# Optimization experiments

Hardware: AMD Instinct MI355X
Metric: run time of the kernel (lower is better)

The kernel has to match this reference:

```python
import jax, jax.numpy as jnp
import numpy as np


def setup_inputs() -> dict:
    key = jax.random.key(0)
    ks = jax.random.split(key, 8)
    B, S, H = 16, 512, 1024
    K, E, L = 32, 1024, 2  # max_node_length, max_edge_length=K**2, num_labels
    seq = jax.random.normal(ks[0], (B, S, H), jnp.float32)
    # structured cumulative proof offsets: col0=1 ('<s>' offset, skipped by forward),
    # then n increasing offsets, zeros terminate. n <= K-1 so NAF node fits in K slots.
    rng = np.random.default_rng(0)
    off = np.zeros((B, K), np.int64)
    off[:, 0] = 1
    for b in range(B):
        n = int(rng.integers(8, K))  # 8..31 segment nodes
        lens = rng.integers(4, 14, size=n)
        off[b, 1:n + 1] = np.cumsum(lens)  # max < 31*13+1 < S
    s = 0.02
    w = lambda k, shp: jax.random.normal(k, shp, jnp.float32) * s
    return {
        'sequence_outputs': seq,
        'proof_offsets': jnp.asarray(off),
        'naf_W': w(ks[1], (H, H)), 'naf_b': jnp.zeros((H,), jnp.float32),
        'cls_dense_W': w(ks[2], (H, H)), 'cls_dense_b': jnp.zeros((H,), jnp.float32),
        'cls_out_W': w(ks[3], (H, L)), 'cls_out_b': jnp.zeros((L,), jnp.float32),
        'node_dense_W': w(ks[4], (H, H)), 'node_dense_b': jnp.zeros((H,), jnp.float32),
        'node_out_W': w(ks[5], (H, L)), 'node_out_b': jnp.zeros((L,), jnp.float32),
        'edge_dense_W': w(ks[6], (3 * H, H)), 'edge_dense_b': jnp.zeros((H,), jnp.float32),
        'edge_out_W': w(ks[7], (H, L)), 'edge_out_b': jnp.zeros((L,), jnp.float32),
        'max_node_length': K,
        'max_edge_length': E,
    }


def _head(x, dW, db, oW, ob):
    # dropout is identity in eval mode
    return jnp.tanh(x @ dW + db) @ oW + ob


def reference(sequence_outputs, proof_offsets,
              naf_W, naf_b, cls_dense_W, cls_dense_b, cls_out_W, cls_out_b,
              node_dense_W, node_dense_b, node_out_W, node_out_b,
              edge_dense_W, edge_dense_b, edge_out_W, edge_out_b,
              max_node_length, max_edge_length):
    B, S, H = sequence_outputs.shape
    K = max_node_length
    E = max_edge_length
    cls_tok = sequence_outputs[:, 0, :]                      # [B,H]
    naf = cls_tok @ naf_W + naf_b                            # [B,H]
    logits = _head(cls_tok, cls_dense_W, cls_dense_b, cls_out_W, cls_out_b)  # [B,L]

    # segment-mean pooling over variable-length spans
    off = proof_offsets[:, 1:]                               # [B,K-1] cumulative offsets
    valid = off > 0                                          # [B,K-1]
    n = valid.sum(axis=1)                                    # [B] #segment nodes
    starts = jnp.concatenate([jnp.ones((B, 1), off.dtype), off[:, :-1] + 1], axis=1)
    pos = jnp.arange(S)
    mask = ((pos[None, None, :] >= starts[:, :, None])
            & (pos[None, None, :] <= off[:, :, None])
            & valid[:, :, None]).astype(sequence_outputs.dtype)  # [B,K-1,S]
    sums = jnp.einsum('bks,bsh->bkh', mask, sequence_outputs)
    counts = mask.sum(axis=-1, keepdims=True)
    node_emb = sums / jnp.maximum(counts, 1.0)               # [B,K-1,H]

    # place segment nodes in slots [0,n), NAF at slot n, zeros after (padded batch buffer)
    slots = jnp.arange(K)
    is_naf = slots[None, :] == n[:, None]
    is_node = slots[None, :] < n[:, None]
    node_emb_p = jnp.pad(node_emb, ((0, 0), (0, 1), (0, 0)))  # [B,K,H]
    full_nodes = jnp.where(is_naf[:, :, None], naf[:, None, :],
                           jnp.where(is_node[:, :, None], node_emb_p, 0.0))  # [B,K,H]

    node_logits = _head(full_nodes, node_dense_W, node_dense_b, node_out_W, node_out_b)

    # pairwise edge features, row-major flattened per sample with m=n+1 nodes:
    # edge[i*m+j] = [node[j], node[i], node[j]-node[i]]
    m = n + 1                                                # [B]
    e = jnp.arange(E)
    i_idx = e[None, :] // m[:, None]                         # [B,E]
    j_idx = e[None, :] % m[:, None]
    valid_e = e[None, :] < (m * m)[:, None]
    i_c = jnp.clip(i_idx, 0, K - 1)
    j_c = jnp.clip(j_idx, 0, K - 1)
    ni = jnp.take_along_axis(full_nodes, i_c[:, :, None], axis=1)  # [B,E,H]
    nj = jnp.take_along_axis(full_nodes, j_c[:, :, None], axis=1)
    edge_feat = jnp.where(valid_e[:, :, None],
                          jnp.concatenate([nj, ni, nj - ni], axis=-1), 0.0)  # [B,E,3H]

    edge_logits = _head(edge_feat, edge_dense_W, edge_dense_b, edge_out_W, edge_out_b)

    return logits, node_logits, edge_logits
```

## Files before the change

### kernel.cpp

```cpp
#include <hip/hip_runtime.h>
#include <hip/hip_bf16.h>

typedef __hip_bfloat16 bf16;
typedef unsigned short ushort;
typedef __attribute__((ext_vector_type(8))) short short8v;
typedef __attribute__((ext_vector_type(4))) float float4v;

__device__ __forceinline__ float us2f(unsigned int u) {
    union { unsigned int i; float f; } c; c.i = u << 16; return c.f;
}
__device__ __forceinline__ bf16 f2bf(float x) { return __float2bfloat16(x); }
__device__ __forceinline__ ushort f2bfu(float x) {
    union { float f; unsigned int i; } c; c.f = x;
    unsigned int lsb = (c.i >> 16) & 1;
    return (ushort)((c.i + 0x7FFF + lsb) >> 16);
}
__device__ __forceinline__ float fcf(float x) {
    return fminf(1000.f, fmaxf(-1000.f, x));
}
__device__ __forceinline__ int iclamp(int v, int lo, int hi) {
    return v < lo ? lo : (v > hi ? hi : v);
}

__device__ __forceinline__ int po_ps(const int* po) {
    return ((po[1] | po[3] | po[5]) == 0) ? 2 : 1;
}
__device__ __forceinline__ int count_n(const int* po, int b, int ps) {
    int n = 0;
    #pragma unroll
    for (int j = 1; j < 32; ++j) n += (po[(b * 32 + j) * ps] > 0) ? 1 : 0;
    return iclamp(n, 0, 31);
}

__global__ __launch_bounds__(256) void k_sentinel(float* __restrict__ out, int nv, float val) {
    int i = blockIdx.x * 256 + threadIdx.x;
    if (i < nv) out[i] = val;
}


__device__ __forceinline__ void dev_prep(int kt, int nt, int z, int tid,
                                         const float* __restrict__ ndW,
                                         const float* __restrict__ eW,
                                         ushort* __restrict__ Wct, float* smemf)
{
    float (*T)[33] = (float (*)[33])smemf;

    const int k_loc = tid >> 3, n0 = (tid & 7) * 4;
    const size_t gofs = (size_t)(kt * 32 + k_loc) * 1024 + nt * 32 + n0;
    float4 v;
    if (z == 0) {
        v = *(const float4*)(ndW + gofs);
    } else if (z == 1) {
        float4 a = *(const float4*)(eW + gofs);
        float4 b = *(const float4*)(eW + (size_t)2048 * 1024 + gofs);
        v = make_float4(a.x + b.x, a.y + b.y, a.z + b.z, a.w + b.w);
    } else {
        float4 a = *(const float4*)(eW + (size_t)1024 * 1024 + gofs);
        float4 b = *(const float4*)(eW + (size_t)2048 * 1024 + gofs);
        v = make_float4(a.x - b.x, a.y - b.y, a.z - b.z, a.w - b.w);
    }
    T[k_loc][n0 + 0] = v.x; T[k_loc][n0 + 1] = v.y;
    T[k_loc][n0 + 2] = v.z; T[k_loc][n0 + 3] = v.w;
    __syncthreads();

    const int n_loc = tid >> 3, k0 = (tid & 7) * 4;
    ushort* dst = Wct + (size_t)z * 1024 * 1024 + (size_t)(nt * 32 + n_loc) * 1024 + kt * 32 + k0;
    ushort4 o;
    o.x = f2bfu(T[k0 + 0][n_loc]); o.y = f2bfu(T[k0 + 1][n_loc]);
    o.z = f2bfu(T[k0 + 2][n_loc]); o.w = f2bfu(T[k0 + 3][n_loc]);
    *(ushort4*)dst = o;
}

__device__ __forceinline__ void dev_nodes(int bx, int tid,
                                          const float* __restrict__ seq,
                                          const int* __restrict__ po,
                                          bf16* __restrict__ fn, int bbase)
{
    const int b_loc = bx >> 5;
    const int k = bx & 31;
    const int b = bbase + b_loc;
    const int ps = po_ps(po);
    const int n = count_n(po, b, ps);
    if (k == n) return;

    const int h0 = tid * 4;
    float4 acc = make_float4(0.f, 0.f, 0.f, 0.f);
    if (k < n) {
        int s_end   = iclamp(po[(b * 32 + k + 1) * ps], 1, 511);
        int s_begin = (k == 0) ? 1 : iclamp(po[(b * 32 + k) * ps] + 1, 1, 511);
        if (s_end < s_begin) s_end = s_begin;
        const float inv = 1.0f / (float)(s_end - s_begin + 1);
        float4 acc2 = make_float4(0.f, 0.f, 0.f, 0.f);
        int s = s_begin;
        const float* base = seq + (size_t)b * 524288 + h0;
        for (; s + 1 <= s_end; s += 2) {
            float4 u = *(const float4*)(base + (size_t)s * 1024);
            float4 v = *(const float4*)(base + (size_t)(s + 1) * 1024);
            acc.x += u.x;  acc.y += u.y;  acc.z += u.z;  acc.w += u.w;
            acc2.x += v.x; acc2.y += v.y; acc2.z += v.z; acc2.w += v.w;
        }
        if (s <= s_end) {
            float4 u = *(const float4*)(base + (size_t)s * 1024);
            acc.x += u.x; acc.y += u.y; acc.z += u.z; acc.w += u.w;
        }
        acc.x = (acc.x + acc2.x) * inv; acc.y = (acc.y + acc2.y) * inv;
        acc.z = (acc.z + acc2.z) * inv; acc.w = (acc.w + acc2.w) * inv;
    }
    bf16* dst = fn + (size_t)(b_loc * 32 + k) * 1024 + h0;
    dst[0] = f2bf(acc.x); dst[1] = f2bf(acc.y); dst[2] = f2bf(acc.z); dst[3] = f2bf(acc.w);
}

__device__ __forceinline__ void dev_cls(int b_loc, int q, int tid,
                                        const float* __restrict__ seq,
                                        const int* __restrict__ po,
                                        const float* __restrict__ nafW, const float* __restrict__ nafb,
                                        const float* __restrict__ clsW, const float* __restrict__ clsb,
                                        const float* __restrict__ clsoW,
                                        bf16* __restrict__ fn,
                                        float* __restrict__ cacc,
                                        int bbase, float* smemf)
{
    const int b = bbase + b_loc;
    float* xs   = smemf;
    float* redc = smemf + 1024;
    float* redn = smemf + 2048;
    for (int j = tid; j < 1024; j += 256) xs[j] = seq[(size_t)b * 524288 + j];
    __syncthreads();

    const int c16 = tid & 15, kq = tid >> 4;
    const int col0 = q * 64 + c16 * 4;
    const int kb = kq * 64;
    const float* wc_base = clsW + (size_t)kb * 1024 + col0;
    const float* wn_base = nafW + (size_t)kb * 1024 + col0;
    float4 ac = make_float4(0.f, 0.f, 0.f, 0.f);
    float4 an = make_float4(0.f, 0.f, 0.f, 0.f);
    #pragma unroll 4
    for (int i = 0; i < 64; ++i) {
        const float x = xs[kb + i];
        float4 wc = *(const float4*)(wc_base + (size_t)i * 1024);
        float4 wn = *(const float4*)(wn_base + (size_t)i * 1024);
        ac.x = fmaf(x, wc.x, ac.x); ac.y = fmaf(x, wc.y, ac.y);
        ac.z = fmaf(x, wc.z, ac.z); ac.w = fmaf(x, wc.w, ac.w);
        an.x = fmaf(x, wn.x, an.x); an.y = fmaf(x, wn.y, an.y);
        an.z = fmaf(x, wn.z, an.z); an.w = fmaf(x, wn.w, an.w);
    }
    *(float4*)&redc[kq * 64 + c16 * 4] = ac;
    *(float4*)&redn[kq * 64 + c16 * 4] = an;
    __syncthreads();

    if (tid < 64) {
        const int cl = tid;
        float cs = 0.f, ns = 0.f;
        #pragma unroll
        for (int kk = 0; kk < 16; ++kk) {
            cs += redc[kk * 64 + cl];
            ns += redn[kk * 64 + cl];
        }
        const int hout = q * 64 + cl;
        const int ps = po_ps(po);
        const int n = count_n(po, b, ps);
        fn[(size_t)(b_loc * 32 + n) * 1024 + hout] = f2bf(ns + nafb[hout]);
        float h = tanhf(cs + clsb[hout]);
        float2 ow = ((const float2*)clsoW)[hout];
        float q0 = h * ow.x, q1 = h * ow.y;
        #pragma unroll
        for (int off = 32; off > 0; off >>= 1) {
            q0 += __shfl_down(q0, off, 64);
            q1 += __shfl_down(q1, off, 64);
        }
        if (cl == 0) {
            cacc[(b_loc * 16 + q) * 2 + 0] = q0;
            cacc[(b_loc * 16 + q) * 2 + 1] = q1;
        }
    }
}

__device__ __forceinline__ void dev_econ(int tid,
                                         const float* __restrict__ edb,
                                         const float* __restrict__ eoW,
                                         float* __restrict__ econ)
{
    if (tid >= 64) return;
    const int lane = tid;
    float a0 = 0.f, a1 = 0.f;
    #pragma unroll
    for (int c = 0; c < 16; ++c) {
        const int idx = c * 64 + lane;
        float t = tanhf(edb[idx]);
        float2 ow = ((const float2*)eoW)[idx];
        a0 = fmaf(t, ow.x, a0);
        a1 = fmaf(t, ow.y, a1);
    }
    #pragma unroll
    for (int off = 32; off > 0; off >>= 1) {
        a0 += __shfl_down(a0, off, 64);
        a1 += __shfl_down(a1, off, 64);
    }
    if (lane == 0) { econ[0] = a0; econ[1] = a1; }
}

__global__ __launch_bounds__(256) void k_fusedA(const float* __restrict__ seq,
                                                const int* __restrict__ po,
                                                const float* __restrict__ nafW, const float* __restrict__ nafb,
                                                const float* __restrict__ clsW, const float* __restrict__ clsb,
                                                const float* __restrict__ clsoW,
                                                const float* __restrict__ ndW,
                                                const float* __restrict__ eW,
                                                const float* __restrict__ edb,
                                                const float* __restrict__ eoW,
                                                bf16* __restrict__ fn,
                                                float* __restrict__ cacc,
                                                ushort* __restrict__ Wct,
                                                float* __restrict__ econ)
{
    __shared__ __align__(16) float smem[3072];
    const int blk = blockIdx.x;
    const int tid = threadIdx.x;
    if (blk < 256) {
        dev_cls(blk & 15, blk >> 4, tid, seq, po, nafW, nafb, clsW, clsb, clsoW, fn, cacc, 0, smem);
    } else if (blk < 768) {
        dev_nodes(blk - 256, tid, seq, po, fn, 0);
    } else if (blk < 3840) {
        const int rem = blk - 768;
        const int z = rem >> 10, t10 = rem & 1023;
        dev_prep(t10 & 31, t10 >> 5, z, tid, ndW, eW, Wct, smem);
    } else {
        dev_econ(tid, edb, eoW, econ);
    }
}

__global__ __launch_bounds__(256) void k_nodes(const float* __restrict__ seq,
                                               const int* __restrict__ po,
                                               bf16* __restrict__ fn, int bbase)
{
    dev_nodes(blockIdx.x, threadIdx.x, seq, po, fn, bbase);
}
__global__ __launch_bounds__(256) void k_cls(const float* __restrict__ seq,
                                             const int* __restrict__ po,
                                             const float* __restrict__ nafW, const float* __restrict__ nafb,
                                             const float* __restrict__ clsW, const float* __restrict__ clsb,
                                             const float* __restrict__ clsoW,
                                             bf16* __restrict__ fn,
                                             float* __restrict__ cacc, int bbase)
{
    __shared__ __align__(16) float smem[3072];
    dev_cls(blockIdx.x, blockIdx.y, threadIdx.x, seq, po, nafW, nafb, clsW, clsb, clsoW, fn, cacc, bbase, smem);
}

__global__ __launch_bounds__(256) void k_huv_mfma(const bf16* __restrict__ X,
                                                  const ushort* __restrict__ Wct,
                                                  const float* __restrict__ ndb,
                                                  const float* __restrict__ noW,
                                                  float* __restrict__ nacc,
                                                  bf16* __restrict__ U,
                                                  bf16* __restrict__ V)
{
    const int rt = blockIdx.x;
    const int cc = blockIdx.y;
    const int z  = blockIdx.z;
    const int tid = threadIdx.x;
    const int w = tid >> 6, lane = tid & 63;
    const int quad = lane >> 4, l16 = lane & 15;
    const int rbase = rt * 16;

    __shared__ char smem[32768];
    short* A_lds = (short*)smem;
    float* Rs    = (float*)smem;

    {
        const int r = tid >> 4, s = tid & 15;
        const ushort* src = (const ushort*)X + (size_t)(rbase + r) * 1024 + s * 64;
        #pragma unroll
        for (int cch = 0; cch < 8; ++cch) {
            const int k0 = s * 64 + cch * 8;
            uint4 v = *(const uint4*)(src + cch * 8);
            const int slot = ((k0 >> 5) * 64 + ((k0 >> 3) & 3) * 16 + r) * 8;
            *(uint4*)&A_lds[slot] = v;
        }
    }
    __syncthreads();

    const ushort* Wz = Wct + (size_t)z * 1024 * 1024;
    const int nbase = cc * 128 + w * 32;
    const ushort* B0 = Wz + (size_t)(nbase + l16) * 1024 + quad * 8;
    const ushort* B1 = B0 + (size_t)16 * 1024;

    float4v acc0 = {0.f, 0.f, 0.f, 0.f};
    float4v acc1 = {0.f, 0.f, 0.f, 0.f};

    #pragma unroll 4
    for (int ks = 0; ks < 1024; ks += 32) {
        short8v a  = *(const short8v*)&A_lds[((ks >> 5) * 64 + quad * 16 + l16) * 8];
        short8v b0 = *(const short8v*)(B0 + ks);
        short8v b1 = *(const short8v*)(B1 + ks);
        acc0 = __builtin_amdgcn_mfma_f32_16x16x32_bf16(a, b0, acc0, 0, 0, 0);
        acc1 = __builtin_amdgcn_mfma_f32_16x16x32_bf16(a, b1, acc1, 0, 0, 0);
    }
    __syncthreads();

    #pragma unroll
    for (int reg = 0; reg < 4; ++reg) {
        Rs[(quad * 4 + reg) * 128 + w * 32 + l16]      = acc0[reg];
        Rs[(quad * 4 + reg) * 128 + w * 32 + 16 + l16] = acc1[reg];
    }
    __syncthreads();

    const int row = tid >> 4;
    const int c0 = (tid & 15) * 8;
    const int gcol0 = cc * 128 + c0;
    const float* src = &Rs[row * 128 + c0];
    float s[8];
    {
        float4 a = ((const float4*)src)[0];
        float4 b = ((const float4*)src)[1];
        s[0] = a.x; s[1] = a.y; s[2] = a.z; s[3] = a.w;
        s[4] = b.x; s[5] = b.y; s[6] = b.z; s[7] = b.w;
    }
    if (z == 0) {
        float q0 = 0.f, q1 = 0.f;
        #pragma unroll
        for (int e = 0; e < 8; ++e) {
            float t = tanhf(s[e] + ndb[gcol0 + e]);
            float2 ow = ((const float2*)noW)[gcol0 + e];
            q0 = fmaf(t, ow.x, q0);
            q1 = fmaf(t, ow.y, q1);
        }
        #pragma unroll
        for (int off = 8; off > 0; off >>= 1) {
            q0 += __shfl_down(q0, off, 16);
            q1 += __shfl_down(q1, off, 16);
        }
        if ((tid & 15) == 0) {
            float* np = nacc + ((size_t)(rbase + row) * 8 + cc) * 2;
            np[0] = q0; np[1] = q1;
        }
    } else {
        bf16* dstbuf = (z == 1) ? U : V;
        bf16* dst = dstbuf + (size_t)(rbase + row) * 1024 + gcol0;
        #pragma unroll
        for (int e = 0; e < 8; ++e) dst[e] = f2bf(s[e]);
    }
}

__global__ __launch_bounds__(256) void k_huv_valu(const bf16* __restrict__ X,
                                                  const float* __restrict__ ndW, const float* __restrict__ ndb,
                                                  const float* __restrict__ noW,
                                                  const float* __restrict__ eW,
                                                  float* __restrict__ nacc,
                                                  bf16* __restrict__ U,
                                                  bf16* __restrict__ V)
{
    const int rt = blockIdx.x, cc = blockIdx.y, z = blockIdx.z;
    const int tid = threadIdx.x;
    const int w = tid >> 6, lane = tid & 63;
    const int rg = lane >> 4, cg = lane & 15;
    const int rbase = rt * 16;
    const int colb = cc * 128 + cg * 8;

    __shared__ float LDSb[8192];
    float* Xs = LDSb;
    float* Rs = LDSb;

    const float* W0;
    const float* W1 = nullptr;
    float sgn = 1.f;
    if (z == 0)      { W0 = ndW; }
    else if (z == 1) { W0 = eW; W1 = eW + (size_t)2048 * 1024; }
    else             { W0 = eW + (size_t)1024 * 1024; W1 = eW + (size_t)2048 * 1024; sgn = -1.f; }

    float acc[32];
    #pragma unroll
    for (int i = 0; i < 32; ++i) acc[i] = 0.f;

    const int sr = tid & 15, sq0 = tid >> 4;
    const ushort* Xu = (const ushort*)X;

    for (int ks = 0; ks < 1024; ks += 256) {
        __syncthreads();
        #pragma unroll
        for (int it = 0; it < 4; ++it) {
            int qq = sq0 + it * 16;
            ushort4 xv = *(const ushort4*)(Xu + (size_t)(rbase + sr) * 1024 + ks + qq * 4);
            int kk = qq * 4;
            Xs[(kk + 0) * 16 + sr] = us2f(xv.x);
            Xs[(kk + 1) * 16 + sr] = us2f(xv.y);
            Xs[(kk + 2) * 16 + sr] = us2f(xv.z);
            Xs[(kk + 3) * 16 + sr] = us2f(xv.w);
        }
        __syncthreads();
        const int k0 = ks + w * 64;
        for (int kk = 0; kk < 64; ++kk) {
            float4 xv = *(const float4*)&Xs[(w * 64 + kk) * 16 + rg * 4];
            const float* wp0 = W0 + (size_t)(k0 + kk) * 1024 + colb;
            float4 wa = ((const float4*)wp0)[0];
            float4 wb = ((const float4*)wp0)[1];
            if (W1) {
                const float* wp1 = W1 + (size_t)(k0 + kk) * 1024 + colb;
                float4 va = ((const float4*)wp1)[0];
                float4 vb = ((const float4*)wp1)[1];
                wa.x = fmaf(sgn, va.x, wa.x); wa.y = fmaf(sgn, va.y, wa.y);
                wa.z = fmaf(sgn, va.z, wa.z); wa.w = fmaf(sgn, va.w, wa.w);
                wb.x = fmaf(sgn, vb.x, wb.x); wb.y = fmaf(sgn, vb.y, wb.y);
                wb.z = fmaf(sgn, vb.z, wb.z); wb.w = fmaf(sgn, vb.w, wb.w);
            }
            float xr[4] = {xv.x, xv.y, xv.z, xv.w};
            #pragma unroll
            for (int rr = 0; rr < 4; ++rr) {
                acc[rr*8+0] = fmaf(xr[rr], wa.x, acc[rr*8+0]);
                acc[rr*8+1] = fmaf(xr[rr], wa.y, acc[rr*8+1]);
                acc[rr*8+2] = fmaf(xr[rr], wa.z, acc[rr*8+2]);
                acc[rr*8+3] = fmaf(xr[rr], wa.w, acc[rr*8+3]);
                acc[rr*8+4] = fmaf(xr[rr], wb.x, acc[rr*8+4]);
                acc[rr*8+5] = fmaf(xr[rr], wb.y, acc[rr*8+5]);
                acc[rr*8+6] = fmaf(xr[rr], wb.z, acc[rr*8+6]);
                acc[rr*8+7] = fmaf(xr[rr], wb.w, acc[rr*8+7]);
            }
        }
    }
    __syncthreads();
    #pragma unroll
    for (int rr = 0; rr < 4; ++rr) {
        float* dst = &Rs[w * 2048 + (rg * 4 + rr) * 128 + cg * 8];
        *(float4*)(dst)     = make_float4(acc[rr*8+0], acc[rr*8+1], acc[rr*8+2], acc[rr*8+3]);
        *(float4*)(dst + 4) = make_float4(acc[rr*8+4], acc[rr*8+5], acc[rr*8+6], acc[rr*8+7]);
    }
    __syncthreads();
    const int row = tid >> 4;
    const int c0 = (tid & 15) * 8;
    float s[8];
    #pragma unroll
    for (int e = 0; e < 8; ++e) s[e] = 0.f;
    #pragma unroll
    for (int ww = 0; ww < 4; ++ww) {
        const float* src = &Rs[ww * 2048 + row * 128 + c0];
        float4 a = ((const float4*)src)[0];
        float4 b = ((const float4*)src)[1];
        s[0] += a.x; s[1] += a.y; s[2] += a.z; s[3] += a.w;
        s[4] += b.x; s[5] += b.y; s[6] += b.z; s[7] += b.w;
    }
    const int gcol0 = cc * 128 + c0;
    if (z == 0) {
        float q0 = 0.f, q1 = 0.f;
        #pragma unroll
        for (int e = 0; e < 8; ++e) {
            float t = tanhf(s[e] + ndb[gcol0 + e]);
            float2 ow = ((const float2*)noW)[gcol0 + e];
            q0 = fmaf(t, ow.x, q0);
            q1 = fmaf(t, ow.y, q1);
        }
        #pragma unroll
        for (int off = 8; off > 0; off >>= 1) {
            q0 += __shfl_down(q0, off, 16);
            q1 += __shfl_down(q1, off, 16);
        }
        if ((tid & 15) == 0) {
            float* np = nacc + ((size_t)(rbase + row) * 8 + cc) * 2;
            np[0] = q0; np[1] = q1;
        }
    } else {
        bf16* dstbuf = (z == 1) ? U : V;
        bf16* dst = dstbuf + (size_t)(rbase + row) * 1024 + gcol0;
        #pragma unroll
        for (int e = 0; e < 8; ++e) dst[e] = f2bf(s[e]);
    }
}

__global__ __launch_bounds__(256) void k_fin2(const float* __restrict__ nacc,
                                              const float* __restrict__ cacc,
                                              const float* __restrict__ nob,
                                              const float* __restrict__ clsob,
                                              float* __restrict__ out,
                                              int bbase, int nb)
{
    const int idx = blockIdx.x * 256 + threadIdx.x;
    const int R = nb * 32;
    if (idx < R) {
        const float4* p = (const float4*)(nacc + (size_t)idx * 16);
        float4 a = p[0], b4 = p[1], c4 = p[2], d4 = p[3];
        float s0 = a.x + a.z + b4.x + b4.z + c4.x + c4.z + d4.x + d4.z;
        float s1 = a.y + a.w + b4.y + b4.w + c4.y + c4.w + d4.y + d4.w;
        out[32 + bbase * 64 + idx * 2 + 0] = fcf(s0 + nob[0]);
        out[32 + bbase * 64 + idx * 2 + 1] = fcf(s1 + nob[1]);
    } else if (idx < R + nb * 2) {
        const int c = idx - R;
        const int b = c >> 1, l = c & 1;
        float s = 0.f;
        for (int q = 0; q < 16; ++q) s += cacc[(b * 16 + q) * 2 + l];
        out[(bbase + b) * 2 + l] = fcf(s + clsob[l]);
    }
}

__global__ __launch_bounds__(256) void k_edge(const bf16* __restrict__ U,
                                              const bf16* __restrict__ V,
                                              const float* __restrict__ edb,
                                              const float* __restrict__ eoW, const float* __restrict__ eob,
                                              const int* __restrict__ po,
                                              float* __restrict__ out,
                                              int bbase)
{
    const int blk = blockIdx.x;
    const int b_loc = blk >> 8;
    const int b = bbase + b_loc;
    const int tid = threadIdx.x;
    const int w = tid >> 6, lane = tid & 63;
    const int e = (blk & 255) * 4 + w;
    const int ps = po_ps(po);
    const int n = count_n(po, b, ps);
    const int m = n + 1;
    const bool valid = e < m * m;
    int i = 0, j = 0;
    if (valid) { i = e / m; j = e - i * m; }
    i = iclamp(i, 0, 31); j = iclamp(j, 0, 31);

    const ushort* urow = (const ushort*)U + (size_t)(b_loc * 32 + j) * 1024;
    const ushort* vrow = (const ushort*)V + (size_t)(b_loc * 32 + i) * 1024;

    float a0 = 0.f, a1 = 0.f;
    #pragma unroll
    for (int c = 0; c < 16; ++c) {
        const int idx = c * 64 + lane;
        float p = edb[idx];
        if (valid) p += us2f(urow[idx]) + us2f(vrow[idx]);
        float t = tanhf(p);
        float2 ow = ((const float2*)eoW)[idx];
        a0 = fmaf(t, ow.x, a0);
        a1 = fmaf(t, ow.y, a1);
    }
    #pragma unroll
    for (int off = 32; off > 0; off >>= 1) {
        a0 += __shfl_down(a0, off, 64);
        a1 += __shfl_down(a1, off, 64);
    }
    if (lane == 0) {
        const size_t o = 32 + 1024 + (size_t)(b * 1024 + e) * 2;
        out[o + 0] = fcf(a0 + eob[0]);
        out[o + 1] = fcf(a1 + eob[1]);
    }
}

__global__ __launch_bounds__(256) void k_fusedC(const bf16* __restrict__ U,
                                                const bf16* __restrict__ V,
                                                const float* __restrict__ nacc,
                                                const float* __restrict__ cacc,
                                                const float* __restrict__ nob,
                                                const float* __restrict__ clsob,
                                                const float* __restrict__ edb,
                                                const float* __restrict__ eoW,
                                                const float* __restrict__ eob,
                                                const float* __restrict__ econ,
                                                const int* __restrict__ po,
                                                float* __restrict__ out)
{
    const int blk = blockIdx.x;
    const int tid = threadIdx.x;

    if (blk >= 4096) {
        const int idx = (blk - 4096) * 256 + tid;
        if (idx < 512) {
            const float4* p = (const float4*)(nacc + (size_t)idx * 16);
            float4 a = p[0], b4 = p[1], c4 = p[2], d4 = p[3];
            float s0 = a.x + a.z + b4.x + b4.z + c4.x + c4.z + d4.x + d4.z;
            float s1 = a.y + a.w + b4.y + b4.w + c4.y + c4.w + d4.y + d4.w;
            out[32 + idx * 2 + 0] = fcf(s0 + nob[0]);
            out[32 + idx * 2 + 1] = fcf(s1 + nob[1]);
        } else if (idx < 544) {
            const int c = idx - 512;
            const int b = c >> 1, l = c & 1;
            float s = 0.f;
            for (int q = 0; q < 16; ++q) s += cacc[(b * 16 + q) * 2 + l];
            out[b * 2 + l] = fcf(s + clsob[l]);
        }
        return;
    }

    const int b = blk >> 8;
    const int w = tid >> 6, lane = tid & 63;
    const int e = (blk & 255) * 4 + w;
    const int ps = po_ps(po);
    const int n = count_n(po, b, ps);
    const int m = n + 1;
    const size_t o = 32 + 1024 + (size_t)(b * 1024 + e) * 2;

    if (e >= m * m) {
        if (lane == 0) {
            out[o + 0] = fcf(econ[0] + eob[0]);
            out[o + 1] = fcf(econ[1] + eob[1]);
        }
        return;
    }

    int i = e / m, j = e - i * m;
    i = iclamp(i, 0, 31); j = iclamp(j, 0, 31);
    const ushort* urow = (const ushort*)U + (size_t)(b * 32 + j) * 1024;
    const ushort* vrow = (const ushort*)V + (size_t)(b * 32 + i) * 1024;

    float a0 = 0.f, a1 = 0.f;
    #pragma unroll
    for (int c = 0; c < 16; ++c) {
        const int idx = c * 64 + lane;
        float p = edb[idx] + us2f(urow[idx]) + us2f(vrow[idx]);
        float t = tanhf(p);
        float2 ow = ((const float2*)eoW)[idx];
        a0 = fmaf(t, ow.x, a0);
        a1 = fmaf(t, ow.y, a1);
    }
    #pragma unroll
    for (int off = 32; off > 0; off >>= 1) {
        a0 += __shfl_down(a0, off, 64);
        a1 += __shfl_down(a1, off, 64);
    }
    if (lane == 0) {
        out[o + 0] = fcf(a0 + eob[0]);
        out[o + 1] = fcf(a1 + eob[1]);
    }
}

extern "C" void kernel_launch(void* const* d_in, const int* in_sizes, int n_in,
                              void* d_out, int out_size, void* d_ws, size_t ws_size,
                              hipStream_t stream) {
    (void)out_size;
    float* out = (float*)d_out;

    bool ok = (n_in >= 16)
        && in_sizes[0] == 8388608 && in_sizes[1] == 512
        && in_sizes[2] == 1048576 && in_sizes[3] == 1024
        && in_sizes[4] == 1048576 && in_sizes[5] == 1024
        && in_sizes[6] == 2048    && in_sizes[7] == 2
        && in_sizes[8] == 1048576 && in_sizes[9] == 1024
        && in_sizes[10] == 2048   && in_sizes[11] == 2
        && in_sizes[12] == 3145728 && in_sizes[13] == 1024
        && in_sizes[14] == 2048   && in_sizes[15] == 2;
    if (!ok) {
        hipLaunchKernelGGL(k_sentinel, dim3(133), dim3(256), 0, stream, out, 33824, 111.0f);
        return;
    }

    const float* seq   = (const float*)d_in[0];
    const int*   po    = (const int*)d_in[1];
    const float* nafW  = (const float*)d_in[2];
    const float* nafb  = (const float*)d_in[3];
    const float* clsW  = (const float*)d_in[4];
    const float* clsb  = (const float*)d_in[5];
    const float* clsoW = (const float*)d_in[6];
    const float* clsob = (const float*)d_in[7];
    const float* ndW   = (const float*)d_in[8];
    const float* ndb   = (const float*)d_in[9];
    const float* noW   = (const float*)d_in[10];
    const float* nob   = (const float*)d_in[11];
    const float* eW    = (const float*)d_in[12];
    const float* edb   = (const float*)d_in[13];
    const float* eoW   = (const float*)d_in[14];
    const float* eob   = (const float*)d_in[15];

    char* ws = (char*)d_ws;

    const size_t fnB   = (size_t)512 * 1024 * 2;
    const size_t naccB = (size_t)512 * 8 * 2 * sizeof(float);
    const size_t caccB = (size_t)16 * 16 * 2 * sizeof(float);
    const size_t econB = 64;
    const size_t wctB  = (size_t)3 * 1024 * 1024 * 2;
    const size_t needA = 3 * fnB + naccB + caccB + econB + wctB;
    const size_t needB = 3 * fnB + naccB + caccB;
    const size_t fnC   = (size_t)32 * 1024 * 2;
    const size_t needC = 3 * fnC + (size_t)32 * 8 * 2 * sizeof(float) + (size_t)16 * 2 * sizeof(float);

    if (ws_size >= needA) {
        bf16*   fn   = (bf16*)(ws);
        bf16*   U    = (bf16*)(ws + fnB);
        bf16*   V    = (bf16*)(ws + 2 * fnB);
        float*  nacc = (float*)(ws + 3 * fnB);
        float*  cacc = (float*)(ws + 3 * fnB + naccB);
        float*  econ = (float*)(ws + 3 * fnB + naccB + caccB);
        ushort* Wct  = (ushort*)(ws + 3 * fnB + naccB + caccB + econB);
        hipLaunchKernelGGL(k_fusedA, dim3(3841), dim3(256), 0, stream,
                           seq, po, nafW, nafb, clsW, clsb, clsoW, ndW, eW, edb, eoW,
                           fn, cacc, Wct, econ);
        hipLaunchKernelGGL(k_huv_mfma, dim3(32, 8, 3), dim3(256), 0, stream,
                           fn, Wct, ndb, noW, nacc, U, V);
        hipLaunchKernelGGL(k_fusedC, dim3(4099), dim3(256), 0, stream,
                           U, V, nacc, cacc, nob, clsob, edb, eoW, eob, econ, po, out);
    } else if (ws_size >= needB) {
        bf16*  fn   = (bf16*)(ws);
        bf16*  U    = (bf16*)(ws + fnB);
        bf16*  V    = (bf16*)(ws + 2 * fnB);
        float* nacc = (float*)(ws + 3 * fnB);
        float* cacc = (float*)(ws + 3 * fnB + naccB);
        hipLaunchKernelGGL(k_nodes, dim3(512), dim3(256), 0, stream, seq, po, fn, 0);
        hipLaunchKernelGGL(k_cls, dim3(16, 16), dim3(256), 0, stream,
                           seq, po, nafW, nafb, clsW, clsb, clsoW, fn, cacc, 0);
        hipLaunchKernelGGL(k_huv_valu, dim3(32, 8, 3), dim3(256), 0, stream,
                           fn, ndW, ndb, noW, eW, nacc, U, V);
        hipLaunchKernelGGL(k_fin2, dim3(3), dim3(256), 0, stream, nacc, cacc, nob, clsob, out, 0, 16);
        hipLaunchKernelGGL(k_edge, dim3(4096), dim3(256), 0, stream,
                           U, V, edb, eoW, eob, po, out, 0);
    } else if (ws_size >= needC) {
        bf16*  fn   = (bf16*)(ws);
        bf16*  U    = (bf16*)(ws + fnC);
        bf16*  V    = (bf16*)(ws + 2 * fnC);
        float* nacc = (float*)(ws + 3 * fnC);
        float* cacc = nacc + 32 * 8 * 2;
        for (int b = 0; b < 16; ++b) {
            hipLaunchKernelGGL(k_nodes, dim3(32), dim3(256), 0, stream, seq, po, fn, b);
            hipLaunchKernelGGL(k_cls, dim3(1, 16), dim3(256), 0, stream,
                               seq, po, nafW, nafb, clsW, clsb, clsoW, fn, cacc, b);
            hipLaunchKernelGGL(k_huv_valu, dim3(2, 8, 3), dim3(256), 0, stream,
                               fn, ndW, ndb, noW, eW, nacc, U, V);
            hipLaunchKernelGGL(k_fin2, dim3(1), dim3(256), 0, stream, nacc, cacc, nob, clsob, out, b, 1);
            hipLaunchKernelGGL(k_edge, dim3(256), dim3(256), 0, stream,
                               U, V, edb, eoW, eob, po, out, b);
        }
    } else {
        hipLaunchKernelGGL(k_sentinel, dim3(133), dim3(256), 0, stream, out, 33824, 222.0f);
    }
}
```

Baseline: 179.8 us.

## Coarsen weight prep, enlarge MFMA row tile, vectorize edge loads, reorder fused blocks

Several independent changes. The weight transpose/convert prep now handles four k-tiles per block, cutting the block count. The MFMA GEMM takes 32 rows per block with four accumulators so each B fragment is reused twice, and the grid is halved. Node mean pooling unrolls by four, the edge kernel loads U/V/bias as wide contiguous vectors per lane instead of strided scalars, and node blocks are scheduled before cls blocks. Risks are fewer blocks giving lower occupancy and larger shared memory per block.

```diff
diff --git a/kernel.cpp b/kernel.cpp
--- a/kernel.cpp
+++ b/kernel.cpp
@@ -38,37 +38,44 @@
 }
 
 
-__device__ __forceinline__ void dev_prep(int kt, int nt, int z, int tid,
-                                         const float* __restrict__ ndW,
-                                         const float* __restrict__ eW,
-                                         ushort* __restrict__ Wct, float* smemf)
-{
-    float (*T)[33] = (float (*)[33])smemf;
-
+__device__ __forceinline__ void dev_prep4(int nt, int kg, int z, int tid,
+                                          const float* __restrict__ ndW,
+                                          const float* __restrict__ eW,
+                                          ushort* __restrict__ Wct, float* smemf)
+{
     const int k_loc = tid >> 3, n0 = (tid & 7) * 4;
-    const size_t gofs = (size_t)(kt * 32 + k_loc) * 1024 + nt * 32 + n0;
-    float4 v;
-    if (z == 0) {
-        v = *(const float4*)(ndW + gofs);
-    } else if (z == 1) {
-        float4 a = *(const float4*)(eW + gofs);
-        float4 b = *(const float4*)(eW + (size_t)2048 * 1024 + gofs);
-        v = make_float4(a.x + b.x, a.y + b.y, a.z + b.z, a.w + b.w);
-    } else {
-        float4 a = *(const float4*)(eW + (size_t)1024 * 1024 + gofs);
-        float4 b = *(const float4*)(eW + (size_t)2048 * 1024 + gofs);
-        v = make_float4(a.x - b.x, a.y - b.y, a.z - b.z, a.w - b.w);
-    }
-    T[k_loc][n0 + 0] = v.x; T[k_loc][n0 + 1] = v.y;
-    T[k_loc][n0 + 2] = v.z; T[k_loc][n0 + 3] = v.w;
+    const size_t colofs = (size_t)nt * 32 + n0;
+    float4 va[4], vb[4];
+    #pragma unroll
+    for (int t = 0; t < 4; ++t) {
+        const int kt = kg * 4 + t;
+        const size_t gofs = (size_t)(kt * 32 + k_loc) * 1024 + colofs;
+        if (z == 0)      va[t] = *(const float4*)(ndW + gofs);
+        else if (z == 1) va[t] = *(const float4*)(eW + gofs);
+        else             va[t] = *(const float4*)(eW + (size_t)1024 * 1024 + gofs);
+        if (z != 0)      vb[t] = *(const float4*)(eW + (size_t)2048 * 1024 + gofs);
+    }
+    #pragma unroll
+    for (int t = 0; t < 4; ++t) {
+        float4 v = va[t];
+        if (z == 1) { v.x += vb[t].x; v.y += vb[t].y; v.z += vb[t].z; v.w += vb[t].w; }
+        else if (z == 2) { v.x -= vb[t].x; v.y -= vb[t].y; v.z -= vb[t].z; v.w -= vb[t].w; }
+        float* T = smemf + t * 1056 + k_loc * 33 + n0;
+        T[0] = v.x; T[1] = v.y; T[2] = v.z; T[3] = v.w;
+    }
     __syncthreads();
 
     const int n_loc = tid >> 3, k0 = (tid & 7) * 4;
-    ushort* dst = Wct + (size_t)z * 1024 * 1024 + (size_t)(nt * 32 + n_loc) * 1024 + kt * 32 + k0;
-    ushort4 o;
-    o.x = f2bfu(T[k0 + 0][n_loc]); o.y = f2bfu(T[k0 + 1][n_loc]);
-    o.z = f2bfu(T[k0 + 2][n_loc]); o.w = f2bfu(T[k0 + 3][n_loc]);
-    *(ushort4*)dst = o;
+    #pragma unroll
+    for (int t = 0; t < 4; ++t) {
+        const int kt = kg * 4 + t;
+        const float* T = smemf + t * 1056;
+        ushort* dst = Wct + (size_t)z * 1024 * 1024 + (size_t)(nt * 32 + n_loc) * 1024 + kt * 32 + k0;
+        ushort4 o;
+        o.x = f2bfu(T[(k0 + 0) * 33 + n_loc]); o.y = f2bfu(T[(k0 + 1) * 33 + n_loc]);
+        o.z = f2bfu(T[(k0 + 2) * 33 + n_loc]); o.w = f2bfu(T[(k0 + 3) * 33 + n_loc]);
+        *(ushort4*)dst = o;
+    }
 }
 
 __device__ __forceinline__ void dev_nodes(int bx, int tid,
@@ -84,30 +91,38 @@
     if (k == n) return;
 
     const int h0 = tid * 4;
-    float4 acc = make_float4(0.f, 0.f, 0.f, 0.f);
+    float4 a0 = make_float4(0.f, 0.f, 0.f, 0.f);
     if (k < n) {
         int s_end   = iclamp(po[(b * 32 + k + 1) * ps], 1, 511);
         int s_begin = (k == 0) ? 1 : iclamp(po[(b * 32 + k) * ps] + 1, 1, 511);
         if (s_end < s_begin) s_end = s_begin;
         const float inv = 1.0f / (float)(s_end - s_begin + 1);
-        float4 acc2 = make_float4(0.f, 0.f, 0.f, 0.f);
+        float4 a1 = make_float4(0.f, 0.f, 0.f, 0.f);
+        float4 a2 = make_float4(0.f, 0.f, 0.f, 0.f);
+        float4 a3 = make_float4(0.f, 0.f, 0.f, 0.f);
+        const float* base = seq + (size_t)b * 524288 + h0;
         int s = s_begin;
-        const float* base = seq + (size_t)b * 524288 + h0;
-        for (; s + 1 <= s_end; s += 2) {
+        for (; s + 3 <= s_end; s += 4) {
+            float4 u0 = *(const float4*)(base + (size_t)(s + 0) * 1024);
+            float4 u1 = *(const float4*)(base + (size_t)(s + 1) * 1024);
+            float4 u2 = *(const float4*)(base + (size_t)(s + 2) * 1024);
+            float4 u3 = *(const float4*)(base + (size_t)(s + 3) * 1024);
+            a0.x += u0.x; a0.y += u0.y; a0.z += u0.z; a0.w += u0.w;
+            a1.x += u1.x; a1.y += u1.y; a1.z += u1.z; a1.w += u1.w;
+            a2.x += u2.x; a2.y += u2.y; a2.z += u2.z; a2.w += u2.w;
+            a3.x += u3.x; a3.y += u3.y; a3.z += u3.z; a3.w += u3.w;
+        }
+        for (; s <= s_end; ++s) {
             float4 u = *(const float4*)(base + (size_t)s * 1024);
-            float4 v = *(const float4*)(base + (size_t)(s + 1) * 1024);
-            acc.x += u.x;  acc.y += u.y;  acc.z += u.z;  acc.w += u.w;
-            acc2.x += v.x; acc2.y += v.y; acc2.z += v.z; acc2.w += v.w;
-        }
-        if (s <= s_end) {
-            float4 u = *(const float4*)(base + (size_t)s * 1024);
-            acc.x += u.x; acc.y += u.y; acc.z += u.z; acc.w += u.w;
-        }
-        acc.x = (acc.x + acc2.x) * inv; acc.y = (acc.y + acc2.y) * inv;
-        acc.z = (acc.z + acc2.z) * inv; acc.w = (acc.w + acc2.w) * inv;
+            a0.x += u.x; a0.y += u.y; a0.z += u.z; a0.w += u.w;
+        }
+        a0.x = (a0.x + a1.x + a2.x + a3.x) * inv;
+        a0.y = (a0.y + a1.y + a2.y + a3.y) * inv;
+        a0.z = (a0.z + a1.z + a2.z + a3.z) * inv;
+        a0.w = (a0.w + a1.w + a2.w + a3.w) * inv;
     }
     bf16* dst = fn + (size_t)(b_loc * 32 + k) * 1024 + h0;
-    dst[0] = f2bf(acc.x); dst[1] = f2bf(acc.y); dst[2] = f2bf(acc.z); dst[3] = f2bf(acc.w);
+    dst[0] = f2bf(a0.x); dst[1] = f2bf(a0.y); dst[2] = f2bf(a0.z); dst[3] = f2bf(a0.w);
 }
 
 __device__ __forceinline__ void dev_cls(int b_loc, int q, int tid,
@@ -213,17 +228,18 @@
                                                 ushort* __restrict__ Wct,
                                                 float* __restrict__ econ)
 {
-    __shared__ __align__(16) float smem[3072];
+    __shared__ __align__(16) float smem[4224];
     const int blk = blockIdx.x;
     const int tid = threadIdx.x;
-    if (blk < 256) {
-        dev_cls(blk & 15, blk >> 4, tid, seq, po, nafW, nafb, clsW, clsb, clsoW, fn, cacc, 0, smem);
+    if (blk < 512) {
+        dev_nodes(blk, tid, seq, po, fn, 0);
     } else if (blk < 768) {
-        dev_nodes(blk - 256, tid, seq, po, fn, 0);
-    } else if (blk < 3840) {
+        const int r = blk - 512;
+        dev_cls(r & 15, r >> 4, tid, seq, po, nafW, nafb, clsW, clsb, clsoW, fn, cacc, 0, smem);
+    } else if (blk < 1536) {
         const int rem = blk - 768;
-        const int z = rem >> 10, t10 = rem & 1023;
-        dev_prep(t10 & 31, t10 >> 5, z, tid, ndW, eW, Wct, smem);
+        const int z = rem >> 8, t8 = rem & 255;
+        dev_prep4(t8 >> 3, t8 & 7, z, tid, ndW, eW, Wct, smem);
     } else {
         dev_econ(tid, edb, eoW, econ);
     }
@@ -243,7 +259,7 @@
                                              bf16* __restrict__ fn,
                                              float* __restrict__ cacc, int bbase)
 {
-    __shared__ __align__(16) float smem[3072];
+    __shared__ __align__(16) float smem[4224];
     dev_cls(blockIdx.x, blockIdx.y, threadIdx.x, seq, po, nafW, nafb, clsW, clsb, clsoW, fn, cacc, bbase, smem);
 }
 
@@ -261,20 +277,20 @@
     const int tid = threadIdx.x;
     const int w = tid >> 6, lane = tid & 63;
     const int quad = lane >> 4, l16 = lane & 15;
-    const int rbase = rt * 16;
-
-    __shared__ char smem[32768];
+    const int rbase = rt * 32;
+
+    __shared__ char smem[65536];
     short* A_lds = (short*)smem;
     float* Rs    = (float*)smem;
 
     {
-        const int r = tid >> 4, s = tid & 15;
-        const ushort* src = (const ushort*)X + (size_t)(rbase + r) * 1024 + s * 64;
-        #pragma unroll
-        for (int cch = 0; cch < 8; ++cch) {
-            const int k0 = s * 64 + cch * 8;
+        const int r = tid >> 3, s = tid & 7;
+        const ushort* src = (const ushort*)X + (size_t)(rbase + r) * 1024 + s * 128;
+        #pragma unroll
+        for (int cch = 0; cch < 16; ++cch) {
+            const int k0 = s * 128 + cch * 8;
             uint4 v = *(const uint4*)(src + cch * 8);
-            const int slot = ((k0 >> 5) * 64 + ((k0 >> 3) & 3) * 16 + r) * 8;
+            const int slot = ((k0 >> 5) * 128 + ((k0 >> 3) & 3) * 32 + r) * 8;
             *(uint4*)&A_lds[slot] = v;
         }
     }
@@ -285,60 +301,77 @@
     const ushort* B0 = Wz + (size_t)(nbase + l16) * 1024 + quad * 8;
     const ushort* B1 = B0 + (size_t)16 * 1024;
 
-    float4v acc0 = {0.f, 0.f, 0.f, 0.f};
-    float4v acc1 = {0.f, 0.f, 0.f, 0.f};
+    float4v acc00 = {0.f, 0.f, 0.f, 0.f};
+    float4v acc01 = {0.f, 0.f, 0.f, 0.f};
+    float4v acc10 = {0.f, 0.f, 0.f, 0.f};
+    float4v acc11 = {0.f, 0.f, 0.f, 0.f};
 
     #pragma unroll 4
     for (int ks = 0; ks < 1024; ks += 32) {
-        short8v a  = *(const short8v*)&A_lds[((ks >> 5) * 64 + quad * 16 + l16) * 8];
+        const int sbase = (ks >> 5) * 128 + quad * 32;
+        short8v a0 = *(const short8v*)&A_lds[(sbase + l16) * 8];
+        short8v a1 = *(const short8v*)&A_lds[(sbase + 16 + l16) * 8];
         short8v b0 = *(const short8v*)(B0 + ks);
         short8v b1 = *(const short8v*)(B1 + ks);
-        acc0 = __builtin_amdgcn_mfma_f32_16x16x32_bf16(a, b0, acc0, 0, 0, 0);
-        acc1 = __builtin_amdgcn_mfma_f32_16x16x32_bf16(a, b1, acc1, 0, 0, 0);
+        acc00 = __builtin_amdgcn_mfma_f32_16x16x32_bf16(a0, b0, acc00, 0, 0, 0);
+        acc01 = __builtin_amdgcn_mfma_f32_16x16x32_bf16(a0, b1, acc01, 0, 0, 0);
+        acc10 = __builtin_amdgcn_mfma_f32_16x16x32_bf16(a1, b0, acc10, 0, 0, 0);
+        acc11 = __builtin_amdgcn_mfma_f32_16x16x32_bf16(a1, b1, acc11, 0, 0, 0);
     }
     __syncthreads();
 
     #pragma unroll
     for (int reg = 0; reg < 4; ++reg) {
-        Rs[(quad * 4 + reg) * 128 + w * 32 + l16]      = acc0[reg];
-        Rs[(quad * 4 + reg) * 128 + w * 32 + 16 + l16] = acc1[reg];
+        const int r0 = quad * 4 + reg;
+        Rs[r0 * 128 + w * 32 + l16]             = acc00[reg];
+        Rs[r0 * 128 + w * 32 + 16 + l16]        = acc01[reg];
+        Rs[(16 + r0) * 128 + w * 32 + l16]      = acc10[reg];
+        Rs[(16 + r0) * 128 + w * 32 + 16 + l16] = acc11[reg];
     }
     __syncthreads();
 
-    const int row = tid >> 4;
-    const int c0 = (tid & 15) * 8;
+    const int row = tid >> 3;
+    const int c0 = (tid & 7) * 16;
     const int gcol0 = cc * 128 + c0;
     const float* src = &Rs[row * 128 + c0];
-    float s[8];
+    float s[16];
     {
-        float4 a = ((const float4*)src)[0];
-        float4 b = ((const float4*)src)[1];
-        s[0] = a.x; s[1] = a.y; s[2] = a.z; s[3] = a.w;
-        s[4] = b.x; s[5] = b.y; s[6] = b.z; s[7] = b.w;
+        float4 p0 = ((const float4*)src)[0];
+        float4 p1 = ((const float4*)src)[1];
+        float4 p2 = ((const float4*)src)[2];
+        float4 p3 = ((const float4*)src)[3];
+        s[0]=p0.x; s[1]=p0.y; s[2]=p0.z; s[3]=p0.w;
+        s[4]=p1.x; s[5]=p1.y; s[6]=p1.z; s[7]=p1.w;
+        s[8]=p2.x; s[9]=p2.y; s[10]=p2.z; s[11]=p2.w;
+        s[12]=p3.x; s[13]=p3.y; s[14]=p3.z; s[15]=p3.w;
     }
     if (z == 0) {
         float q0 = 0.f, q1 = 0.f;
         #pragma unroll
-        for (int e = 0; e < 8; ++e) {
+        for (int e = 0; e < 16; ++e) {
             float t = tanhf(s[e] + ndb[gcol0 + e]);
             float2 ow = ((const float2*)noW)[gcol0 + e];
             q0 = fmaf(t, ow.x, q0);
             q1 = fmaf(t, ow.y, q1);
         }
         #pragma unroll
-        for (int off = 8; off > 0; off >>= 1) {
-            q0 += __shfl_down(q0, off, 16);
-            q1 += __shfl_down(q1, off, 16);
-        }
-        if ((tid & 15) == 0) {
+        for (int off = 4; off > 0; off >>= 1) {
+            q0 += __shfl_down(q0, off, 8);
+            q1 += __shfl_down(q1, off, 8);
+        }
+        if ((tid & 7) == 0) {
             float* np = nacc + ((size_t)(rbase + row) * 8 + cc) * 2;
             np[0] = q0; np[1] = q1;
         }
     } else {
         bf16* dstbuf = (z == 1) ? U : V;
-        bf16* dst = dstbuf + (size_t)(rbase + row) * 1024 + gcol0;
-        #pragma unroll
-        for (int e = 0; e < 8; ++e) dst[e] = f2bf(s[e]);
+        ushort* dst = (ushort*)dstbuf + (size_t)(rbase + row) * 1024 + gcol0;
+        ushort4 o0, o1, o2, o3;
+        o0.x=f2bfu(s[0]);  o0.y=f2bfu(s[1]);  o0.z=f2bfu(s[2]);  o0.w=f2bfu(s[3]);
+        o1.x=f2bfu(s[4]);  o1.y=f2bfu(s[5]);  o1.z=f2bfu(s[6]);  o1.w=f2bfu(s[7]);
+        o2.x=f2bfu(s[8]);  o2.y=f2bfu(s[9]);  o2.z=f2bfu(s[10]); o2.w=f2bfu(s[11]);
+        o3.x=f2bfu(s[12]); o3.y=f2bfu(s[13]); o3.z=f2bfu(s[14]); o3.w=f2bfu(s[15]);
+        ((ushort4*)dst)[0]=o0; ((ushort4*)dst)[1]=o1; ((ushort4*)dst)[2]=o2; ((ushort4*)dst)[3]=o3;
     }
 }
 
@@ -594,13 +627,36 @@
     const ushort* urow = (const ushort*)U + (size_t)(b * 32 + j) * 1024;
     const ushort* vrow = (const ushort*)V + (size_t)(b * 32 + i) * 1024;
 
+    const int base = lane * 16;
+    uint4 uu0 = *(const uint4*)(urow + base);
+    uint4 uu1 = *(const uint4*)(urow + base + 8);
+    uint4 vv0 = *(const uint4*)(vrow + base);
+    uint4 vv1 = *(const uint4*)(vrow + base + 8);
+    float4 eb0 = ((const float4*)(edb + base))[0];
+    float4 eb1 = ((const float4*)(edb + base))[1];
+    float4 eb2 = ((const float4*)(edb + base))[2];
+    float4 eb3 = ((const float4*)(edb + base))[3];
+    const float* ebp = (const float*)&eb0;
+    float ebv[16];
+    ebv[0]=eb0.x; ebv[1]=eb0.y; ebv[2]=eb0.z; ebv[3]=eb0.w;
+    ebv[4]=eb1.x; ebv[5]=eb1.y; ebv[6]=eb1.z; ebv[7]=eb1.w;
+    ebv[8]=eb2.x; ebv[9]=eb2.y; ebv[10]=eb2.z; ebv[11]=eb2.w;
+    ebv[12]=eb3.x; ebv[13]=eb3.y; ebv[14]=eb3.z; ebv[15]=eb3.w;
+    (void)ebp;
+    const ushort* up = (const ushort*)&uu0;
+    const ushort* up1 = (const ushort*)&uu1;
+    const ushort* vp = (const ushort*)&vv0;
+    const ushort* vp1 = (const ushort*)&vv1;
+    const float2* ow2 = (const float2*)eoW + base;
+
     float a0 = 0.f, a1 = 0.f;
     #pragma unroll
     for (int c = 0; c < 16; ++c) {
-        const int idx = c * 64 + lane;
-        float p = edb[idx] + us2f(urow[idx]) + us2f(vrow[idx]);
+        const ushort uc = (c < 8) ? up[c] : up1[c - 8];
+        const ushort vc = (c < 8) ? vp[c] : vp1[c - 8];
+        float p = ebv[c] + us2f(uc) + us2f(vc);
         float t = tanhf(p);
-        float2 ow = ((const float2*)eoW)[idx];
+        float2 ow = ow2[c];
         a0 = fmaf(t, ow.x, a0);
         a1 = fmaf(t, ow.y, a1);
     }
@@ -672,10 +728,10 @@
         float*  cacc = (float*)(ws + 3 * fnB + naccB);
         float*  econ = (float*)(ws + 3 * fnB + naccB + caccB);
         ushort* Wct  = (ushort*)(ws + 3 * fnB + naccB + caccB + econB);
-        hipLaunchKernelGGL(k_fusedA, dim3(3841), dim3(256), 0, stream,
+        hipLaunchKernelGGL(k_fusedA, dim3(1537), dim3(256), 0, stream,
                            seq, po, nafW, nafb, clsW, clsb, clsoW, ndW, eW, edb, eoW,
                            fn, cacc, Wct, econ);
-        hipLaunchKernelGGL(k_huv_mfma, dim3(32, 8, 3), dim3(256), 0, stream,
+        hipLaunchKernelGGL(k_huv_mfma, dim3(16, 8, 3), dim3(256), 0, stream,
                            fn, Wct, ndb, noW, nacc, U, V);
         hipLaunchKernelGGL(k_fusedC, dim3(4099), dim3(256), 0, stream,
                            U, V, nacc, cacc, nob, clsob, edb, eoW, eob, econ, po, out);
```

After: 183.8 us. +2.2%, slower.
